# Optimization experiments

Hardware: AMD Instinct MI355X
Metric: run time of the kernel (lower is better)

The kernel has to match this reference:

```python
import jax, jax.numpy as jnp
import numpy as np

B, N, D, H = 4, 2048, 1024, 16
DH = D // H


def setup_inputs() -> dict:
    key = jax.random.key(0)
    ks = jax.random.split(key, 9)
    std = 0.02
    return {
        "x": jax.random.normal(ks[0], (B, N, D), dtype=jnp.float32),
        "Wq": jax.random.normal(ks[1], (D, D), dtype=jnp.float32) * std,
        "bq": jnp.zeros((D,), dtype=jnp.float32),
        "Wk": jax.random.normal(ks[2], (D, D), dtype=jnp.float32) * std,
        "bk": jnp.zeros((D,), dtype=jnp.float32),
        "Wv": jax.random.normal(ks[3], (D, D), dtype=jnp.float32) * std,
        "bv": jnp.zeros((D,), dtype=jnp.float32),
        "Wo": jax.random.normal(ks[4], (D, D), dtype=jnp.float32) * std,
        "bo": jnp.zeros((D,), dtype=jnp.float32),
        "k": 8,
        "dilation": 2,
    }


def _dilated_mask(n_q, n_k, k, dilation):
    # allowed[i, j] = True iff |j - i| <= k*dilation and (j - i) % dilation == 0
    i = jnp.arange(n_q)[:, None]
    j = jnp.arange(n_k)[None, :]
    d = j - i
    return (jnp.abs(d) <= k * dilation) & ((d % dilation) == 0)


def reference(x, Wq, bq, Wk, bk, Wv, bv, Wo, bo, k, dilation):
    b, n_q, d_model = x.shape
    n_heads = H
    d_head = d_model // n_heads
    # self-attention: context = x
    q = (x @ Wq + bq).reshape(b, n_q, n_heads, d_head).transpose(0, 2, 1, 3)  # (B,H,Nq,Dh)
    kk = (x @ Wk + bk).reshape(b, n_q, n_heads, d_head).transpose(0, 2, 1, 3)
    v = (x @ Wv + bv).reshape(b, n_q, n_heads, d_head).transpose(0, 2, 1, 3)

    scale = 1.0 / np.sqrt(d_head).astype(np.float32)
    scores = jnp.einsum("bhqd,bhkd->bhqk", q, kk) * scale  # (B,H,Nq,Nk)
    allowed = _dilated_mask(n_q, n_q, k, dilation)  # (Nq,Nk)
    scores = jnp.where(allowed[None, None], scores, -jnp.inf)
    attn = jax.nn.softmax(scores, axis=-1)
    out = jnp.einsum("bhqk,bhkd->bhqd", attn, v)  # (B,H,Nq,Dh)
    out = out.transpose(0, 2, 1, 3).reshape(b, n_q, d_model)
    return out @ Wo + bo
```

## Files before the change

### kernel.cpp

```cpp
#include <hip/hip_runtime.h>
#include <hip/hip_bf16.h>
#include <hip/hip_fp16.h>
#include <stdint.h>

using bf16 = __hip_bfloat16;

typedef __bf16    bf16x8 __attribute__((ext_vector_type(8)));
typedef float     floatx4 __attribute__((ext_vector_type(4)));
typedef _Float16  f16x2 __attribute__((ext_vector_type(2)));
typedef _Float16  f16x8 __attribute__((ext_vector_type(8)));

typedef __attribute__((address_space(3))) void as3_void;
typedef __attribute__((address_space(1))) void as1_void;

#define GLD_LDS16(gp, lp) \
  __builtin_amdgcn_global_load_lds((as1_void*)(uintptr_t)(gp), (as3_void*)(uintptr_t)(lp), 16, 0, 0)

#if __has_builtin(__builtin_amdgcn_fdot2)
#define DOT2(a, b, c) __builtin_amdgcn_fdot2((a), (b), (c), false)
#else
#define DOT2(a, b, c) ((c) + (float)(a)[0] * (float)(b)[0] + (float)(a)[1] * (float)(b)[1])
#endif

__global__ __launch_bounds__(256) void prep_kernel(
    const float* __restrict__ x,
    const float* __restrict__ Wq, const float* __restrict__ Wk,
    const float* __restrict__ Wv, const float* __restrict__ Wo,
    bf16* __restrict__ xbf, bf16* __restrict__ WTqkv, bf16* __restrict__ WoT) {
  __shared__ float tile[64 * 68];
  const int blk = blockIdx.x;
  const int tid = threadIdx.x;
  if (blk < 1024) {
    const int z = blk >> 8, t = blk & 255;
    const float* src = (z == 0) ? Wq : (z == 1) ? Wk : (z == 2) ? Wv : Wo;
    bf16* dst = (z < 3) ? (WTqkv + (size_t)z * 1024 * 1024) : WoT;
    const int nbase = (t & 15) * 64, kbase = (t >> 4) * 64;
    const int r1 = tid >> 4, c1 = tid & 15;
#pragma unroll
    for (int it = 0; it < 4; ++it) {
      const int row = r1 + it * 16;
      const float4 v = *(const float4*)(src + (size_t)(kbase + row) * 1024 + nbase + c1 * 4);
      *(float4*)(tile + row * 68 + c1 * 4) = v;
    }
    __syncthreads();
    const int c2 = tid & 7, n2 = tid >> 3;
#pragma unroll
    for (int it2 = 0; it2 < 2; ++it2) {
      const int n = n2 + it2 * 32;
      bf16 o[8];
#pragma unroll
      for (int s = 0; s < 8; ++s) o[s] = (bf16)tile[(8 * c2 + s) * 68 + n];
      *(uint4*)(dst + (size_t)(nbase + n) * 1024 + kbase + 8 * c2) = *(const uint4*)o;
    }
  } else {
    const size_t basei = ((size_t)(blk - 1024) * 256 + tid) * 16;
#pragma unroll
    for (int h = 0; h < 2; ++h) {
      const float4 a = *(const float4*)(x + basei + h * 8);
      const float4 b = *(const float4*)(x + basei + h * 8 + 4);
      bf16 o[8] = {(bf16)a.x, (bf16)a.y, (bf16)a.z, (bf16)a.w,
                   (bf16)b.x, (bf16)b.y, (bf16)b.z, (bf16)b.w};
      *(uint4*)(xbf + basei + h * 8) = *(const uint4*)o;
    }
  }
}

template <int MODE>
__global__ __launch_bounds__(256) void gemm_bt_kernel(
    const bf16* __restrict__ A, const bf16* __restrict__ Bt,
    const float* __restrict__ b0, const float* __restrict__ b1, const float* __restrict__ b2,
    __half* __restrict__ out0, __half* __restrict__ out1, __half* __restrict__ out2,
    float* __restrict__ fout) {
  const int tid  = threadIdx.x;
  const int m0   = blockIdx.x * 128;
  const int n0   = blockIdx.y * 128;
  const int lane = tid & 63;
  const int wave = tid >> 6;
  const int wr   = (wave >> 1) * 64;
  const int wc   = (wave & 1) * 64;
  const int quad = lane >> 4;
  const int l16  = lane & 15;

  __shared__ alignas(16) bf16 As[128 * 64];
  __shared__ alignas(16) bf16 Bs[128 * 64];

  const int srow = tid >> 3;
  const int cg   = (tid & 7) ^ (srow & 7);
  uint64_t aoff;
  if (MODE == 0) {
    aoff = (uint64_t)(m0 + srow) * 1024 + cg * 8;
  } else {
    const int b = m0 >> 11, seq0 = m0 & 2047;
    aoff = (uint64_t)b * 2097152 + (uint64_t)(seq0 + srow) * 64 + cg * 8;
  }
  const uint64_t boff = (uint64_t)(n0 + srow) * 1024 + cg * 8;

  floatx4 acc[4][4];
#pragma unroll
  for (int i = 0; i < 4; ++i)
#pragma unroll
    for (int j = 0; j < 4; ++j) {
      floatx4 z = {0.f, 0.f, 0.f, 0.f};
      acc[i][j] = z;
    }

  for (int k0 = 0; k0 < 1024; k0 += 64) {
    __syncthreads();
#pragma unroll
    for (int it = 0; it < 4; ++it) {
      if (MODE == 0)
        GLD_LDS16(A + aoff + (uint64_t)it * 32768 + k0, (char*)As + it * 4096 + tid * 16);
      else
        GLD_LDS16(A + aoff + (uint64_t)it * 2048 + (uint64_t)(k0 >> 6) * 131072,
                  (char*)As + it * 4096 + tid * 16);
      GLD_LDS16(Bt + boff + (uint64_t)it * 32768 + k0, (char*)Bs + it * 4096 + tid * 16);
    }
    __syncthreads();

#pragma unroll
    for (int kc = 0; kc < 2; ++kc) {
      bf16x8 af[4], bfr[4];
#pragma unroll
      for (int i = 0; i < 4; ++i) {
        const int mrow = wr + i * 16 + l16;
        const int pca  = (kc * 4 + quad) ^ (mrow & 7);
        af[i] = *(const bf16x8*)(As + mrow * 64 + pca * 8);
        const int nrow = wc + i * 16 + l16;
        const int pcb  = (kc * 4 + quad) ^ (nrow & 7);
        bfr[i] = *(const bf16x8*)(Bs + nrow * 64 + pcb * 8);
      }
#pragma unroll
      for (int i = 0; i < 4; ++i)
#pragma unroll
        for (int j = 0; j < 4; ++j)
          acc[i][j] = __builtin_amdgcn_mfma_f32_16x16x32_bf16(af[i], bfr[j], acc[i][j], 0, 0, 0);
    }
  }

#pragma unroll
  for (int i = 0; i < 4; ++i) {
#pragma unroll
    for (int j = 0; j < 4; ++j) {
#pragma unroll
      for (int r = 0; r < 4; ++r) {
        const int m = m0 + wr + i * 16 + quad * 4 + r;
        const int n = n0 + wc + j * 16 + l16;
        float v = acc[i][j][r];
        if (MODE == 0) {
          const int which = n >> 10;
          const int c = n & 1023;
          const float* bp = (which == 0) ? b0 : (which == 1) ? b1 : b2;
          __half* op      = (which == 0) ? out0 : (which == 1) ? out1 : out2;
          v += bp[c];
          const int h = c >> 6, dh = c & 63;
          const int bb = m >> 11, seq = m & 2047;
          op[(uint64_t)(bb * 16 + h) * 131072 + (uint64_t)seq * 64 + dh] = (__half)v;
        } else {
          fout[(uint64_t)m * 1024 + n] = v + b0[n];
        }
      }
    }
  }
}

#define RMAXA 32
#define VTS 176
#define PS  104

__global__ __launch_bounds__(256) void dilated_attn_mfma_kernel(
    const __half* __restrict__ Q, const __half* __restrict__ K, const __half* __restrict__ V,
    bf16* __restrict__ attn_out, const int* __restrict__ kptr, const int* __restrict__ dptr) {
  const int tid  = threadIdx.x;
  const int wave = tid >> 6, lane = tid & 63;
  const int quad = lane >> 4, l16 = lane & 15;
  const int bh = blockIdx.x >> 5;
  const int Q0 = (blockIdx.x & 31) * 64;
  const int kk  = kptr[0];
  const int dil = dptr[0];
  const int R   = kk * dil;
  const size_t base = (size_t)bh * 2048 * 64;
  const _Float16* Qh = (const _Float16*)Q;
  const _Float16* Kh = (const _Float16*)K;
  const _Float16* Vh = (const _Float16*)V;

  __shared__ alignas(16) _Float16 smem[64 * VTS + 4 * 16 * PS];
  _Float16* VT = smem;
  _Float16* Pw = smem + 64 * VTS + wave * 16 * PS;

  const bool fast = (R <= RMAXA) && (dil >= 1);

  if (fast) {
    {
      const int nch = (64 * VTS + 4 * 16 * PS) / 8;
      const f16x8 z = {0, 0, 0, 0, 0, 0, 0, 0};
      for (int c = tid; c < nch; c += 256) ((f16x8*)smem)[c] = z;
    }
    __syncthreads();

    const int jlo = Q0 - R;
    const int lo = (jlo > 0) ? jlo : 0;
    const int hi = (Q0 + 63 + R < 2047) ? Q0 + 63 + R : 2047;
    const int nrows = hi - lo + 1;
    for (int idx = tid; idx < nrows * 8; idx += 256) {
      const int r = idx >> 3, c = idx & 7;
      const int j = lo + r;
      const f16x8 v = *(const f16x8*)(Vh + base + (size_t)j * 64 + c * 8);
      const int col = j - jlo + 32;
#pragma unroll
      for (int s = 0; s < 8; ++s) VT[(c * 8 + s) * VTS + col] = v[s];
    }
    __syncthreads();

    const int i0 = Q0 + wave * 16;
    const f16x8 a0 = *(const f16x8*)(Qh + base + (size_t)(i0 + l16) * 64 + quad * 8);
    const f16x8 a1 = *(const f16x8*)(Qh + base + (size_t)(i0 + l16) * 64 + 32 + quad * 8);

    const int nkt = (16 + 2 * R + 15) >> 4;
    const int jw0 = i0 - R;
    float lsum[4] = {0.f, 0.f, 0.f, 0.f};
    const floatx4 zf = {0.f, 0.f, 0.f, 0.f};

    for (int kt = 0; kt < nkt; ++kt) {
      const int j0 = jw0 + 16 * kt;
      const int jn = j0 + l16;
      const int jc = (jn < 0) ? 0 : (jn > 2047 ? 2047 : jn);
      const f16x8 b0 = *(const f16x8*)(Kh + base + (size_t)jc * 64 + quad * 8);
      const f16x8 b1 = *(const f16x8*)(Kh + base + (size_t)jc * 64 + 32 + quad * 8);
      floatx4 s4 = __builtin_amdgcn_mfma_f32_16x16x32_f16(a0, b0, zf, 0, 0, 0);
      s4 = __builtin_amdgcn_mfma_f32_16x16x32_f16(a1, b1, s4, 0, 0, 0);
#pragma unroll
      for (int r = 0; r < 4; ++r) {
        const int m = quad * 4 + r;
        const int d = jn - (i0 + m);
        const bool valid = ((unsigned)jn < 2048u) && (d >= -R) && (d <= R) && (d % dil == 0);
        const float pe = valid ? __expf(s4[r] * 0.125f) : 0.f;
        lsum[r] += pe;
        Pw[m * PS + kt * 16 + l16] = (_Float16)pe;
      }
    }
#pragma unroll
    for (int r = 0; r < 4; ++r) {
      lsum[r] += __shfl_xor(lsum[r], 1);
      lsum[r] += __shfl_xor(lsum[r], 2);
      lsum[r] += __shfl_xor(lsum[r], 4);
      lsum[r] += __shfl_xor(lsum[r], 8);
    }

    const int nkc = (nkt * 16 + 31) >> 5;
    floatx4 o[4] = {zf, zf, zf, zf};
    const int vbase = 16 * wave + 32;
    for (int c = 0; c < nkc; ++c) {
      const f16x8 pa = *(const f16x8*)(Pw + l16 * PS + c * 32 + quad * 8);
#pragma unroll
      for (int t = 0; t < 4; ++t) {
        const f16x8 vb = *(const f16x8*)(VT + (t * 16 + l16) * VTS + vbase + c * 32 + quad * 8);
        o[t] = __builtin_amdgcn_mfma_f32_16x16x32_f16(pa, vb, o[t], 0, 0, 0);
      }
    }

#pragma unroll
    for (int t = 0; t < 4; ++t) {
#pragma unroll
      for (int r = 0; r < 4; ++r)
        Pw[(quad * 4 + r) * PS + t * 16 + l16] = (_Float16)(o[t][r] / lsum[r]);
    }
    const int orow = lane >> 2, oseg = lane & 3;
#pragma unroll
    for (int hseg = 0; hseg < 2; ++hseg) {
      const f16x8 ov = *(const f16x8*)(Pw + orow * PS + oseg * 16 + hseg * 8);
      bf16 ob[8];
#pragma unroll
      for (int s = 0; s < 8; ++s) ob[s] = (bf16)(float)ov[s];
      *(uint4*)(attn_out + base + (size_t)(i0 + orow) * 64 + oseg * 16 + hseg * 8) =
          *(const uint4*)ob;
    }
    return;
  }

  {
    const int i = Q0 + (tid >> 2);
  }
  if (tid < 64) {
    const int i = Q0 + tid;
    float l = 0.f;
    float oacc[64];
#pragma unroll
    for (int u = 0; u < 64; ++u) oacc[u] = 0.f;
    float qv[64];
#pragma unroll
    for (int u = 0; u < 64; ++u) qv[u] = (float)Qh[base + (size_t)i * 64 + u];
    for (int t = -kk; t <= kk; ++t) {
      const int j = i + (int)((long long)t * dil);
      if (j < 0 || j >= 2048) continue;
      float s = 0.f;
      for (int u = 0; u < 64; ++u) s += qv[u] * (float)Kh[base + (size_t)j * 64 + u];
      const float pe = __expf(s * 0.125f);
      l += pe;
      for (int u = 0; u < 64; ++u) oacc[u] += pe * (float)Vh[base + (size_t)j * 64 + u];
    }
    for (int u = 0; u < 64; ++u)
      attn_out[base + (size_t)i * 64 + u] = (bf16)(oacc[u] / l);
  }
}

extern "C" void kernel_launch(void* const* d_in, const int* in_sizes, int n_in,
                              void* d_out, int out_size, void* d_ws, size_t ws_size,
                              hipStream_t stream) {
  const float* x  = (const float*)d_in[0];
  const float* Wq = (const float*)d_in[1];
  const float* bq = (const float*)d_in[2];
  const float* Wk = (const float*)d_in[3];
  const float* bk = (const float*)d_in[4];
  const float* Wv = (const float*)d_in[5];
  const float* bv = (const float*)d_in[6];
  const float* Wo = (const float*)d_in[7];
  const float* bo = (const float*)d_in[8];
  const int* kp   = (const int*)d_in[9];
  const int* dp   = (const int*)d_in[10];
  float* out = (float*)d_out;

  bf16*   xbf   = (bf16*)d_ws;
  bf16*   WTqkv = xbf + 8388608;
  bf16*   WoT   = WTqkv + 3072 * 1024;
  __half* qbuf  = (__half*)(WoT + 1024 * 1024);
  __half* kbuf  = qbuf + 8388608;
  __half* vbuf  = kbuf + 8388608;
  bf16*   attnH = xbf;

  prep_kernel<<<dim3(3072), 256, 0, stream>>>(x, Wq, Wk, Wv, Wo, xbf, WTqkv, WoT);

  gemm_bt_kernel<0><<<dim3(64, 24), 256, 0, stream>>>(xbf, WTqkv, bq, bk, bv,
                                                      qbuf, kbuf, vbuf, nullptr);

  dilated_attn_mfma_kernel<<<dim3(2048), 256, 0, stream>>>(qbuf, kbuf, vbuf, attnH, kp, dp);

  gemm_bt_kernel<1><<<dim3(64, 8), 256, 0, stream>>>(attnH, WoT, bo, nullptr, nullptr,
                                                     nullptr, nullptr, nullptr, out);
}
```

Baseline: 213.8 us.

## Replace QKV GEMM with 256x256 eight-phase pipelined MFMA kernel

Adds a new QKV projection GEMM that uses 256x256 tiles with 512 threads. It double-buffers swizzled LDS tiles loaded through global_load_lds and interleaves async loads with MFMA phases using explicit barriers, waitcnt and setprio. The goal is to raise data reuse per tile and hide global-load latency behind compute compared with the prior 128x128 kernel. The trade-offs are much larger LDS use (128KB), heavy register pressure from 32 accumulators, and a grid of only 384 blocks, which could leave some of the CUs underused.

```diff
diff --git a/kernel.cpp b/kernel.cpp
--- a/kernel.cpp
+++ b/kernel.cpp
@@ -16,11 +16,10 @@
 #define GLD_LDS16(gp, lp) \
   __builtin_amdgcn_global_load_lds((as1_void*)(uintptr_t)(gp), (as3_void*)(uintptr_t)(lp), 16, 0, 0)
 
-#if __has_builtin(__builtin_amdgcn_fdot2)
-#define DOT2(a, b, c) __builtin_amdgcn_fdot2((a), (b), (c), false)
-#else
-#define DOT2(a, b, c) ((c) + (float)(a)[0] * (float)(b)[0] + (float)(a)[1] * (float)(b)[1])
-#endif
+#define FENCE() asm volatile("" ::: "memory")
+#define BAR()   do { FENCE(); __builtin_amdgcn_s_barrier(); FENCE(); } while (0)
+#define WAITL0() do { asm volatile("s_waitcnt lgkmcnt(0)" ::: "memory"); \
+                      __builtin_amdgcn_sched_barrier(0); } while (0)
 
 __global__ __launch_bounds__(256) void prep_kernel(
     const float* __restrict__ x,
@@ -61,6 +60,173 @@
       bf16 o[8] = {(bf16)a.x, (bf16)a.y, (bf16)a.z, (bf16)a.w,
                    (bf16)b.x, (bf16)b.y, (bf16)b.z, (bf16)b.w};
       *(uint4*)(xbf + basei + h * 8) = *(const uint4*)o;
+    }
+  }
+}
+
+#define SA8(buf, h, kt) do { \
+    GLD_LDS16(A + abase + (uint64_t)((h) * 131072) + (uint64_t)(kt) * 64, \
+              (char*)(&As[(buf)][0]) + (h) * 16384 + ldst); \
+    GLD_LDS16(A + abase + (uint64_t)((h) * 131072 + 65536) + (uint64_t)(kt) * 64, \
+              (char*)(&As[(buf)][0]) + (h) * 16384 + 8192 + ldst); \
+  } while (0)
+
+#define SB8(buf, h, kt) do { \
+    GLD_LDS16(Bt + bbase + (uint64_t)((h) * 131072) + (uint64_t)(kt) * 64, \
+              (char*)(&Bs[(buf)][0]) + (h) * 16384 + ldst); \
+    GLD_LDS16(Bt + bbase + (uint64_t)((h) * 131072 + 65536) + (uint64_t)(kt) * 64, \
+              (char*)(&Bs[(buf)][0]) + (h) * 16384 + 8192 + ldst); \
+  } while (0)
+
+#define RDA8(buf, up) do { \
+    const char* _p = (const char*)(&As[(buf)][0]) + arow0 + (up); \
+    af[0][0] = *(const bf16x8*)(_p + 0 * 2048 + pcb0); \
+    af[0][1] = *(const bf16x8*)(_p + 0 * 2048 + pcb1); \
+    af[1][0] = *(const bf16x8*)(_p + 1 * 2048 + pcb0); \
+    af[1][1] = *(const bf16x8*)(_p + 1 * 2048 + pcb1); \
+    af[2][0] = *(const bf16x8*)(_p + 2 * 2048 + pcb0); \
+    af[2][1] = *(const bf16x8*)(_p + 2 * 2048 + pcb1); \
+    af[3][0] = *(const bf16x8*)(_p + 3 * 2048 + pcb0); \
+    af[3][1] = *(const bf16x8*)(_p + 3 * 2048 + pcb1); \
+  } while (0)
+
+#define RDB8(buf) do { \
+    const char* _p = (const char*)(&Bs[(buf)][0]) + brow0; \
+    bf[0][0] = *(const bf16x8*)(_p + 0 * 2048 + pcb0); \
+    bf[0][1] = *(const bf16x8*)(_p + 0 * 2048 + pcb1); \
+    bf[1][0] = *(const bf16x8*)(_p + 1 * 2048 + pcb0); \
+    bf[1][1] = *(const bf16x8*)(_p + 1 * 2048 + pcb1); \
+    bf[2][0] = *(const bf16x8*)(_p + 2 * 2048 + pcb0); \
+    bf[2][1] = *(const bf16x8*)(_p + 2 * 2048 + pcb1); \
+    bf[3][0] = *(const bf16x8*)(_p + 3 * 2048 + pcb0); \
+    bf[3][1] = *(const bf16x8*)(_p + 3 * 2048 + pcb1); \
+  } while (0)
+
+#define MMQ8(ab, nb) do { \
+    _Pragma("unroll") for (int _i = 0; _i < 4; ++_i) \
+      _Pragma("unroll") for (int _j = 0; _j < 2; ++_j) \
+        _Pragma("unroll") for (int _kc = 0; _kc < 2; ++_kc) \
+          acc[(ab) + _i][(nb) + _j] = __builtin_amdgcn_mfma_f32_16x16x32_bf16( \
+              af[_i][_kc], bf[(nb) + _j][_kc], acc[(ab) + _i][(nb) + _j], 0, 0, 0); \
+  } while (0)
+
+__global__ __launch_bounds__(512, 2) void gemm_qkv_8ph(
+    const bf16* __restrict__ A, const bf16* __restrict__ Bt,
+    const float* __restrict__ b0, const float* __restrict__ b1, const float* __restrict__ b2,
+    __half* __restrict__ out0, __half* __restrict__ out1, __half* __restrict__ out2) {
+  const int t    = threadIdx.x;
+  const int m0   = blockIdx.x * 256;
+  const int n0   = blockIdx.y * 256;
+  const int lane = t & 63;
+  const int wave = t >> 6;
+  const int wm   = wave >> 2;
+  const int wn   = wave & 3;
+  const int quad = lane >> 4;
+  const int l16  = lane & 15;
+
+  __shared__ alignas(16) bf16 As[2][256 * 64];
+  __shared__ alignas(16) bf16 Bs[2][256 * 64];
+
+  const int srt = t >> 3;
+  const int sct = ((t & 7) ^ (srt & 7)) << 3;
+  const uint64_t abase = (uint64_t)(m0 + srt) * 1024 + sct;
+  const uint64_t bbase = (uint64_t)(n0 + srt) * 1024 + sct;
+  const int ldst = t * 16;
+
+  const int arow0 = (wm * 128 + l16) * 128;
+  const int brow0 = (wn * 64 + l16) * 128;
+  const int pcb0  = ((quad) ^ (l16 & 7)) << 4;
+  const int pcb1  = ((4 + quad) ^ (l16 & 7)) << 4;
+
+  floatx4 acc[8][4];
+#pragma unroll
+  for (int i = 0; i < 8; ++i)
+#pragma unroll
+    for (int j = 0; j < 4; ++j) {
+      floatx4 z = {0.f, 0.f, 0.f, 0.f};
+      acc[i][j] = z;
+    }
+  bf16x8 af[4][2], bf[4][2];
+
+  SB8(0, 0, 0); SB8(0, 1, 0); SA8(0, 0, 0); SA8(0, 1, 0);
+  SB8(1, 0, 1); SB8(1, 1, 1); SA8(1, 0, 1);
+  asm volatile("s_waitcnt vmcnt(6)" ::: "memory");
+  BAR();
+
+  for (int i = 0; i < 8; ++i) {
+    const int t1 = 2 * i + 1;
+    const int t2 = 2 * i + 2;
+    const int t3 = 2 * i + 3;
+    const bool pf = (i < 7);
+
+    RDA8(0, 0);
+    RDB8(0);
+    SA8(1, 1, t1);
+    BAR(); WAITL0();
+    __builtin_amdgcn_s_setprio(1); MMQ8(0, 0); __builtin_amdgcn_s_setprio(0);
+    BAR();
+
+    if (pf) SB8(0, 0, t2);
+    BAR();
+    __builtin_amdgcn_s_setprio(1); MMQ8(0, 2); __builtin_amdgcn_s_setprio(0);
+    BAR();
+
+    RDA8(0, 8192);
+    if (pf) SB8(0, 1, t2);
+    BAR(); WAITL0();
+    __builtin_amdgcn_s_setprio(1); MMQ8(4, 0); __builtin_amdgcn_s_setprio(0);
+    BAR();
+
+    if (pf) SA8(0, 0, t2);
+    BAR();
+    __builtin_amdgcn_s_setprio(1); MMQ8(4, 2); __builtin_amdgcn_s_setprio(0);
+    if (pf) { asm volatile("s_waitcnt vmcnt(6)" ::: "memory"); }
+    else    { asm volatile("s_waitcnt vmcnt(0)" ::: "memory"); }
+    BAR();
+
+    RDA8(1, 0);
+    RDB8(1);
+    if (pf) SA8(0, 1, t2);
+    BAR(); WAITL0();
+    __builtin_amdgcn_s_setprio(1); MMQ8(0, 0); __builtin_amdgcn_s_setprio(0);
+    BAR();
+
+    if (pf) SB8(1, 0, t3);
+    BAR();
+    __builtin_amdgcn_s_setprio(1); MMQ8(0, 2); __builtin_amdgcn_s_setprio(0);
+    BAR();
+
+    RDA8(1, 8192);
+    if (pf) SB8(1, 1, t3);
+    BAR(); WAITL0();
+    __builtin_amdgcn_s_setprio(1); MMQ8(4, 0); __builtin_amdgcn_s_setprio(0);
+    BAR();
+
+    if (pf) SA8(1, 0, t3);
+    BAR();
+    __builtin_amdgcn_s_setprio(1); MMQ8(4, 2); __builtin_amdgcn_s_setprio(0);
+    if (pf) { asm volatile("s_waitcnt vmcnt(6)" ::: "memory"); }
+    BAR();
+  }
+
+#pragma unroll
+  for (int mi = 0; mi < 8; ++mi) {
+#pragma unroll
+    for (int ni = 0; ni < 4; ++ni) {
+#pragma unroll
+      for (int r = 0; r < 4; ++r) {
+        const int m = m0 + wm * 128 + mi * 16 + quad * 4 + r;
+        const int n = n0 + wn * 64 + ni * 16 + l16;
+        float v = acc[mi][ni][r];
+        const int which = n >> 10;
+        const int c = n & 1023;
+        const float* bp = (which == 0) ? b0 : (which == 1) ? b1 : b2;
+        __half* op      = (which == 0) ? out0 : (which == 1) ? out1 : out2;
+        v += bp[c];
+        const int h = c >> 6, dh = c & 63;
+        const int bb = m >> 11, seq = m & 2047;
+        op[(uint64_t)(bb * 16 + h) * 131072 + (uint64_t)seq * 64 + dh] = (__half)v;
+      }
     }
   }
 }
@@ -277,9 +443,6 @@
     return;
   }
 
-  {
-    const int i = Q0 + (tid >> 2);
-  }
   if (tid < 64) {
     const int i = Q0 + tid;
     float l = 0.f;
@@ -329,8 +492,8 @@
 
   prep_kernel<<<dim3(3072), 256, 0, stream>>>(x, Wq, Wk, Wv, Wo, xbf, WTqkv, WoT);
 
-  gemm_bt_kernel<0><<<dim3(64, 24), 256, 0, stream>>>(xbf, WTqkv, bq, bk, bv,
-                                                      qbuf, kbuf, vbuf, nullptr);
+  gemm_qkv_8ph<<<dim3(32, 12), 512, 0, stream>>>(xbf, WTqkv, bq, bk, bv,
+                                                 qbuf, kbuf, vbuf);
 
   dilated_attn_mfma_kernel<<<dim3(2048), 256, 0, stream>>>(qbuf, kbuf, vbuf, attnH, kp, dp);
 
```

Result: no change. 214.7 us (+0.4%).

## Replace QKV GEMM with double-buffered 256x192 eight-phase pipelined kernel

Applied to the files above, without the earlier changes.

Replaces the simple 128x128 QKV GEMM with a 512-thread, 256x192-tile kernel. It double-buffers LDS and interleaves global-to-LDS prefetch with MFMA phases, using explicit barriers, waitcnts and setprio. The QKV output becomes a single row-major (B*N, 3072) fp16 buffer written through LDS staging as coalesced 16-byte stores, and the attention and projection kernels read and write this token-major layout directly. The aim is to hide memory latency and avoid scattered 2-byte stores, in exchange for more complex synchronisation and higher LDS and register pressure.

```diff
diff --git a/kernel.cpp b/kernel.cpp
--- a/kernel.cpp
+++ b/kernel.cpp
@@ -7,7 +7,6 @@
 
 typedef __bf16    bf16x8 __attribute__((ext_vector_type(8)));
 typedef float     floatx4 __attribute__((ext_vector_type(4)));
-typedef _Float16  f16x2 __attribute__((ext_vector_type(2)));
 typedef _Float16  f16x8 __attribute__((ext_vector_type(8)));
 
 typedef __attribute__((address_space(3))) void as3_void;
@@ -16,11 +15,10 @@
 #define GLD_LDS16(gp, lp) \
   __builtin_amdgcn_global_load_lds((as1_void*)(uintptr_t)(gp), (as3_void*)(uintptr_t)(lp), 16, 0, 0)
 
-#if __has_builtin(__builtin_amdgcn_fdot2)
-#define DOT2(a, b, c) __builtin_amdgcn_fdot2((a), (b), (c), false)
-#else
-#define DOT2(a, b, c) ((c) + (float)(a)[0] * (float)(b)[0] + (float)(a)[1] * (float)(b)[1])
-#endif
+#define FENCE() asm volatile("" ::: "memory")
+#define BAR()   do { FENCE(); __builtin_amdgcn_s_barrier(); FENCE(); } while (0)
+#define WAITL0() do { asm volatile("s_waitcnt lgkmcnt(0)" ::: "memory"); \
+                      __builtin_amdgcn_sched_barrier(0); } while (0)
 
 __global__ __launch_bounds__(256) void prep_kernel(
     const float* __restrict__ x,
@@ -65,12 +63,174 @@
   }
 }
 
-template <int MODE>
-__global__ __launch_bounds__(256) void gemm_bt_kernel(
+#define SAU(bufi, u, kt) \
+  GLD_LDS16(A + abase + (uint64_t)(u) * 65536 + (uint64_t)(kt) * 64, \
+            (char*)(&As[bufi][0]) + (u) * 8192 + ldst)
+#define SBU(bufi, u, kt) \
+  GLD_LDS16(Bt + bbase + (uint64_t)(u) * 65536 + (uint64_t)(kt) * 64, \
+            (char*)(&Bs[bufi][0]) + (u) * 8192 + ldst)
+
+#define RDA2(bufi, mb) do { \
+    const char* _p = (const char*)(&As[bufi][0]) + (wm * 128 + (mb) * 16 + l16) * 128; \
+    af[0][0] = *(const bf16x8*)(_p + pcb0); \
+    af[0][1] = *(const bf16x8*)(_p + pcb1); \
+    af[1][0] = *(const bf16x8*)(_p + 2048 + pcb0); \
+    af[1][1] = *(const bf16x8*)(_p + 2048 + pcb1); \
+  } while (0)
+
+#define RDB3(bufi) do { \
+    const char* _p = (const char*)(&Bs[bufi][0]) + (wn * 48 + l16) * 128; \
+    bfr[0][0] = *(const bf16x8*)(_p + pcb0); \
+    bfr[0][1] = *(const bf16x8*)(_p + pcb1); \
+    bfr[1][0] = *(const bf16x8*)(_p + 2048 + pcb0); \
+    bfr[1][1] = *(const bf16x8*)(_p + 2048 + pcb1); \
+    bfr[2][0] = *(const bf16x8*)(_p + 4096 + pcb0); \
+    bfr[2][1] = *(const bf16x8*)(_p + 4096 + pcb1); \
+  } while (0)
+
+#define MMQ12(mb) do { \
+    _Pragma("unroll") for (int _i = 0; _i < 2; ++_i) \
+      _Pragma("unroll") for (int _j = 0; _j < 3; ++_j) \
+        _Pragma("unroll") for (int _k = 0; _k < 2; ++_k) \
+          acc[(mb) + _i][_j] = __builtin_amdgcn_mfma_f32_16x16x32_bf16( \
+              af[_i][_k], bfr[_j][_k], acc[(mb) + _i][_j], 0, 0, 0); \
+  } while (0)
+
+__global__ __launch_bounds__(512, 2) void gemm_qkv_8ph(
     const bf16* __restrict__ A, const bf16* __restrict__ Bt,
     const float* __restrict__ b0, const float* __restrict__ b1, const float* __restrict__ b2,
-    __half* __restrict__ out0, __half* __restrict__ out1, __half* __restrict__ out2,
-    float* __restrict__ fout) {
+    __half* __restrict__ qkv) {
+  const int t    = threadIdx.x;
+  const int m0   = blockIdx.x * 256;
+  const int n0   = blockIdx.y * 192;
+  const int lane = t & 63;
+  const int wave = t >> 6;
+  const int wm   = wave >> 2;
+  const int wn   = wave & 3;
+  const int quad = lane >> 4;
+  const int l16  = lane & 15;
+
+  __shared__ alignas(16) bf16 As[2][256 * 64];
+  __shared__ alignas(16) bf16 Bs[2][192 * 64];
+
+  const int srt = t >> 3;
+  const int sct = ((t & 7) ^ (srt & 7)) << 3;
+  const uint64_t abase = (uint64_t)(m0 + srt) * 1024 + sct;
+  const uint64_t bbase = (uint64_t)(n0 + srt) * 1024 + sct;
+  const int ldst = t * 16;
+
+  const int pcb0 = ((quad) ^ (l16 & 7)) << 4;
+  const int pcb1 = ((4 + quad) ^ (l16 & 7)) << 4;
+
+  floatx4 acc[8][3];
+#pragma unroll
+  for (int i = 0; i < 8; ++i)
+#pragma unroll
+    for (int j = 0; j < 3; ++j) {
+      floatx4 z = {0.f, 0.f, 0.f, 0.f};
+      acc[i][j] = z;
+    }
+  bf16x8 af[2][2], bfr[3][2];
+
+  SBU(0, 0, 0); SBU(0, 1, 0); SBU(0, 2, 0);
+  SAU(0, 0, 0); SAU(0, 1, 0); SAU(0, 2, 0); SAU(0, 3, 0);
+  SBU(1, 0, 1); SBU(1, 1, 1); SBU(1, 2, 1);
+  SAU(1, 0, 1); SAU(1, 2, 1);
+  asm volatile("s_waitcnt vmcnt(5)" ::: "memory");
+  BAR();
+
+  for (int i = 0; i < 8; ++i) {
+    const int kt1 = 2 * i + 1;
+    const int kt2 = 2 * i + 2;
+    const int kt3 = 2 * i + 3;
+    const bool pf = (i < 7);
+
+    RDA2(0, 0); RDB3(0);
+    SAU(1, 1, kt1); SAU(1, 3, kt1);
+    BAR(); WAITL0();
+    __builtin_amdgcn_s_setprio(1); MMQ12(0); __builtin_amdgcn_s_setprio(0);
+    BAR();
+
+    RDA2(0, 2);
+    if (pf) { SBU(0, 0, kt2); SBU(0, 1, kt2); }
+    BAR(); WAITL0();
+    __builtin_amdgcn_s_setprio(1); MMQ12(2); __builtin_amdgcn_s_setprio(0);
+    BAR();
+
+    RDA2(0, 4);
+    if (pf) { SBU(0, 2, kt2); SAU(0, 0, kt2); SAU(0, 2, kt2); }
+    BAR(); WAITL0();
+    __builtin_amdgcn_s_setprio(1); MMQ12(4); __builtin_amdgcn_s_setprio(0);
+    BAR();
+
+    RDA2(0, 6);
+    BAR(); WAITL0();
+    __builtin_amdgcn_s_setprio(1); MMQ12(6); __builtin_amdgcn_s_setprio(0);
+    if (pf) { asm volatile("s_waitcnt vmcnt(5)" ::: "memory"); }
+    else    { asm volatile("s_waitcnt vmcnt(0)" ::: "memory"); }
+    BAR();
+
+    RDA2(1, 0); RDB3(1);
+    if (pf) { SAU(0, 1, kt2); SAU(0, 3, kt2); }
+    BAR(); WAITL0();
+    __builtin_amdgcn_s_setprio(1); MMQ12(0); __builtin_amdgcn_s_setprio(0);
+    BAR();
+
+    RDA2(1, 2);
+    if (pf) { SBU(1, 0, kt3); SBU(1, 1, kt3); }
+    BAR(); WAITL0();
+    __builtin_amdgcn_s_setprio(1); MMQ12(2); __builtin_amdgcn_s_setprio(0);
+    BAR();
+
+    RDA2(1, 4);
+    if (pf) { SBU(1, 2, kt3); SAU(1, 0, kt3); SAU(1, 2, kt3); }
+    BAR(); WAITL0();
+    __builtin_amdgcn_s_setprio(1); MMQ12(4); __builtin_amdgcn_s_setprio(0);
+    BAR();
+
+    RDA2(1, 6);
+    BAR(); WAITL0();
+    __builtin_amdgcn_s_setprio(1); MMQ12(6); __builtin_amdgcn_s_setprio(0);
+    if (pf) { asm volatile("s_waitcnt vmcnt(5)" ::: "memory"); }
+    BAR();
+  }
+
+  float bvs[3];
+#pragma unroll
+  for (int nj = 0; nj < 3; ++nj) {
+    const int n = n0 + wn * 48 + nj * 16 + l16;
+    const int which = n >> 10;
+    const int c = n & 1023;
+    bvs[nj] = ((which == 0) ? b0 : (which == 1) ? b1 : b2)[c];
+  }
+  _Float16* stg = (_Float16*)(&As[0][0]);
+#pragma unroll
+  for (int mi = 0; mi < 8; ++mi) {
+#pragma unroll
+    for (int nj = 0; nj < 3; ++nj)
+#pragma unroll
+      for (int r = 0; r < 4; ++r)
+        stg[(wm * 16 + quad * 4 + r) * 200 + wn * 48 + nj * 16 + l16] =
+            (_Float16)(acc[mi][nj][r] + bvs[nj]);
+    BAR();
+#pragma unroll
+    for (int rep = 0; rep < 2; ++rep) {
+      const int cc = t + rep * 512;
+      if (cc < 768) {
+        const int rl = cc / 24;
+        const int ch = cc - rl * 24;
+        const int mrow = m0 + (rl >> 4) * 128 + mi * 16 + (rl & 15);
+        const f16x8 v = *(const f16x8*)(stg + rl * 200 + ch * 8);
+        *(f16x8*)((_Float16*)qkv + (size_t)mrow * 3072 + n0 + ch * 8) = v;
+      }
+    }
+    BAR();
+  }
+}
+
+__global__ __launch_bounds__(256) void gemm_proj(
+    const bf16* __restrict__ A, const bf16* __restrict__ Bt,
+    const float* __restrict__ bias, float* __restrict__ fout) {
   const int tid  = threadIdx.x;
   const int m0   = blockIdx.x * 128;
   const int n0   = blockIdx.y * 128;
@@ -86,13 +246,7 @@
 
   const int srow = tid >> 3;
   const int cg   = (tid & 7) ^ (srow & 7);
-  uint64_t aoff;
-  if (MODE == 0) {
-    aoff = (uint64_t)(m0 + srow) * 1024 + cg * 8;
-  } else {
-    const int b = m0 >> 11, seq0 = m0 & 2047;
-    aoff = (uint64_t)b * 2097152 + (uint64_t)(seq0 + srow) * 64 + cg * 8;
-  }
+  const uint64_t aoff = (uint64_t)(m0 + srow) * 1024 + cg * 8;
   const uint64_t boff = (uint64_t)(n0 + srow) * 1024 + cg * 8;
 
   floatx4 acc[4][4];
@@ -108,11 +262,7 @@
     __syncthreads();
 #pragma unroll
     for (int it = 0; it < 4; ++it) {
-      if (MODE == 0)
-        GLD_LDS16(A + aoff + (uint64_t)it * 32768 + k0, (char*)As + it * 4096 + tid * 16);
-      else
-        GLD_LDS16(A + aoff + (uint64_t)it * 2048 + (uint64_t)(k0 >> 6) * 131072,
-                  (char*)As + it * 4096 + tid * 16);
+      GLD_LDS16(A + aoff + (uint64_t)it * 32768 + k0, (char*)As + it * 4096 + tid * 16);
       GLD_LDS16(Bt + boff + (uint64_t)it * 32768 + k0, (char*)Bs + it * 4096 + tid * 16);
     }
     __syncthreads();
@@ -138,29 +288,15 @@
   }
 
 #pragma unroll
-  for (int i = 0; i < 4; ++i) {
-#pragma unroll
-    for (int j = 0; j < 4; ++j) {
+  for (int i = 0; i < 4; ++i)
+#pragma unroll
+    for (int j = 0; j < 4; ++j)
 #pragma unroll
       for (int r = 0; r < 4; ++r) {
         const int m = m0 + wr + i * 16 + quad * 4 + r;
         const int n = n0 + wc + j * 16 + l16;
-        float v = acc[i][j][r];
-        if (MODE == 0) {
-          const int which = n >> 10;
-          const int c = n & 1023;
-          const float* bp = (which == 0) ? b0 : (which == 1) ? b1 : b2;
-          __half* op      = (which == 0) ? out0 : (which == 1) ? out1 : out2;
-          v += bp[c];
-          const int h = c >> 6, dh = c & 63;
-          const int bb = m >> 11, seq = m & 2047;
-          op[(uint64_t)(bb * 16 + h) * 131072 + (uint64_t)seq * 64 + dh] = (__half)v;
-        } else {
-          fout[(uint64_t)m * 1024 + n] = v + b0[n];
-        }
+        fout[(uint64_t)m * 1024 + n] = acc[i][j][r] + bias[n];
       }
-    }
-  }
 }
 
 #define RMAXA 32
@@ -168,20 +304,20 @@
 #define PS  104
 
 __global__ __launch_bounds__(256) void dilated_attn_mfma_kernel(
-    const __half* __restrict__ Q, const __half* __restrict__ K, const __half* __restrict__ V,
-    bf16* __restrict__ attn_out, const int* __restrict__ kptr, const int* __restrict__ dptr) {
+    const __half* __restrict__ qkv, bf16* __restrict__ attn_out,
+    const int* __restrict__ kptr, const int* __restrict__ dptr) {
   const int tid  = threadIdx.x;
   const int wave = tid >> 6, lane = tid & 63;
   const int quad = lane >> 4, l16 = lane & 15;
   const int bh = blockIdx.x >> 5;
   const int Q0 = (blockIdx.x & 31) * 64;
+  const int b  = bh >> 4, h = bh & 15;
   const int kk  = kptr[0];
   const int dil = dptr[0];
   const int R   = kk * dil;
-  const size_t base = (size_t)bh * 2048 * 64;
-  const _Float16* Qh = (const _Float16*)Q;
-  const _Float16* Kh = (const _Float16*)K;
-  const _Float16* Vh = (const _Float16*)V;
+  const size_t xb = (size_t)b * 2048;
+  const int qo = h * 64, ko = 1024 + h * 64, vo = 2048 + h * 64;
+  const _Float16* Xh = (const _Float16*)qkv;
 
   __shared__ alignas(16) _Float16 smem[64 * VTS + 4 * 16 * PS];
   _Float16* VT = smem;
@@ -204,7 +340,7 @@
     for (int idx = tid; idx < nrows * 8; idx += 256) {
       const int r = idx >> 3, c = idx & 7;
       const int j = lo + r;
-      const f16x8 v = *(const f16x8*)(Vh + base + (size_t)j * 64 + c * 8);
+      const f16x8 v = *(const f16x8*)(Xh + (xb + j) * 3072 + vo + c * 8);
       const int col = j - jlo + 32;
 #pragma unroll
       for (int s = 0; s < 8; ++s) VT[(c * 8 + s) * VTS + col] = v[s];
@@ -212,8 +348,8 @@
     __syncthreads();
 
     const int i0 = Q0 + wave * 16;
-    const f16x8 a0 = *(const f16x8*)(Qh + base + (size_t)(i0 + l16) * 64 + quad * 8);
-    const f16x8 a1 = *(const f16x8*)(Qh + base + (size_t)(i0 + l16) * 64 + 32 + quad * 8);
+    const f16x8 a0 = *(const f16x8*)(Xh + (xb + i0 + l16) * 3072 + qo + quad * 8);
+    const f16x8 a1 = *(const f16x8*)(Xh + (xb + i0 + l16) * 3072 + qo + 32 + quad * 8);
 
     const int nkt = (16 + 2 * R + 15) >> 4;
     const int jw0 = i0 - R;
@@ -224,10 +360,10 @@
       const int j0 = jw0 + 16 * kt;
       const int jn = j0 + l16;
       const int jc = (jn < 0) ? 0 : (jn > 2047 ? 2047 : jn);
-      const f16x8 b0 = *(const f16x8*)(Kh + base + (size_t)jc * 64 + quad * 8);
-      const f16x8 b1 = *(const f16x8*)(Kh + base + (size_t)jc * 64 + 32 + quad * 8);
-      floatx4 s4 = __builtin_amdgcn_mfma_f32_16x16x32_f16(a0, b0, zf, 0, 0, 0);
-      s4 = __builtin_amdgcn_mfma_f32_16x16x32_f16(a1, b1, s4, 0, 0, 0);
+      const f16x8 k0v = *(const f16x8*)(Xh + (xb + jc) * 3072 + ko + quad * 8);
+      const f16x8 k1v = *(const f16x8*)(Xh + (xb + jc) * 3072 + ko + 32 + quad * 8);
+      floatx4 s4 = __builtin_amdgcn_mfma_f32_16x16x32_f16(a0, k0v, zf, 0, 0, 0);
+      s4 = __builtin_amdgcn_mfma_f32_16x16x32_f16(a1, k1v, s4, 0, 0, 0);
 #pragma unroll
       for (int r = 0; r < 4; ++r) {
         const int m = quad * 4 + r;
@@ -271,15 +407,12 @@
       bf16 ob[8];
 #pragma unroll
       for (int s = 0; s < 8; ++s) ob[s] = (bf16)(float)ov[s];
-      *(uint4*)(attn_out + base + (size_t)(i0 + orow) * 64 + oseg * 16 + hseg * 8) =
+      *(uint4*)(attn_out + (xb + i0 + orow) * 1024 + h * 64 + oseg * 16 + hseg * 8) =
           *(const uint4*)ob;
     }
     return;
   }
 
-  {
-    const int i = Q0 + (tid >> 2);
-  }
   if (tid < 64) {
     const int i = Q0 + tid;
     float l = 0.f;
@@ -288,18 +421,18 @@
     for (int u = 0; u < 64; ++u) oacc[u] = 0.f;
     float qv[64];
 #pragma unroll
-    for (int u = 0; u < 64; ++u) qv[u] = (float)Qh[base + (size_t)i * 64 + u];
-    for (int t = -kk; t <= kk; ++t) {
-      const int j = i + (int)((long long)t * dil);
+    for (int u = 0; u < 64; ++u) qv[u] = (float)Xh[(xb + i) * 3072 + qo + u];
+    for (int tt = -kk; tt <= kk; ++tt) {
+      const int j = i + (int)((long long)tt * dil);
       if (j < 0 || j >= 2048) continue;
       float s = 0.f;
-      for (int u = 0; u < 64; ++u) s += qv[u] * (float)Kh[base + (size_t)j * 64 + u];
+      for (int u = 0; u < 64; ++u) s += qv[u] * (float)Xh[(xb + j) * 3072 + ko + u];
       const float pe = __expf(s * 0.125f);
       l += pe;
-      for (int u = 0; u < 64; ++u) oacc[u] += pe * (float)Vh[base + (size_t)j * 64 + u];
+      for (int u = 0; u < 64; ++u) oacc[u] += pe * (float)Xh[(xb + j) * 3072 + vo + u];
     }
     for (int u = 0; u < 64; ++u)
-      attn_out[base + (size_t)i * 64 + u] = (bf16)(oacc[u] / l);
+      attn_out[(xb + i) * 1024 + h * 64 + u] = (bf16)(oacc[u] / l);
   }
 }
 
@@ -322,18 +455,14 @@
   bf16*   xbf   = (bf16*)d_ws;
   bf16*   WTqkv = xbf + 8388608;
   bf16*   WoT   = WTqkv + 3072 * 1024;
-  __half* qbuf  = (__half*)(WoT + 1024 * 1024);
-  __half* kbuf  = qbuf + 8388608;
-  __half* vbuf  = kbuf + 8388608;
-  bf16*   attnH = xbf;
+  __half* qkv   = (__half*)(WoT + 1024 * 1024);
+  bf16*   attnO = xbf;
 
   prep_kernel<<<dim3(3072), 256, 0, stream>>>(x, Wq, Wk, Wv, Wo, xbf, WTqkv, WoT);
 
-  gemm_bt_kernel<0><<<dim3(64, 24), 256, 0, stream>>>(xbf, WTqkv, bq, bk, bv,
-                                                      qbuf, kbuf, vbuf, nullptr);
-
-  dilated_attn_mfma_kernel<<<dim3(2048), 256, 0, stream>>>(qbuf, kbuf, vbuf, attnH, kp, dp);
-
-  gemm_bt_kernel<1><<<dim3(64, 8), 256, 0, stream>>>(attnH, WoT, bo, nullptr, nullptr,
-                                                     nullptr, nullptr, nullptr, out);
+  gemm_qkv_8ph<<<dim3(32, 16), 512, 0, stream>>>(xbf, WTqkv, bq, bk, bv, qkv);
+
+  dilated_attn_mfma_kernel<<<dim3(2048), 256, 0, stream>>>(qkv, attnO, kp, dp);
+
+  gemm_proj<<<dim3(64, 8), 256, 0, stream>>>(attnO, WoT, bo, out);
 }
```

Result: faster. 208.2 us (-2.6%).
